# Performance work log

Hardware: AMD Instinct MI355X
Metric: run time of the kernel (lower is better)

The kernel has to match this reference:

```python
import jax, jax.numpy as jnp
import numpy as np

N = 50000        # nodes
E = 800000       # edges
E_PAIR = 200000  # pos/neg link pairs
IN = 256
HID = (512, 256, 160)
NEG_SLOPE = 0.2


def _lin_w(k, i, o):
    s = 1.0 / np.sqrt(i)
    return jax.random.uniform(k, (i, o), jnp.float32, -s, s)


def setup_inputs() -> dict:
    key = jax.random.key(0)
    ks = jax.random.split(key, 16)
    inp = {
        'x': jax.random.normal(ks[0], (N, IN), jnp.float32),
        'w': jax.random.uniform(ks[1], (E,), jnp.float32),
        'src': jax.random.randint(ks[2], (E,), 0, N),
        'dst': jax.random.randint(ks[3], (E,), 0, N),
        'pos_src': jax.random.randint(ks[4], (E_PAIR,), 0, N),
        'pos_dst': jax.random.randint(ks[5], (E_PAIR,), 0, N),
        'neg_src': jax.random.randint(ks[6], (E_PAIR,), 0, N),
        'neg_dst': jax.random.randint(ks[7], (E_PAIR,), 0, N),
        # GraphConv weights/biases
        'W1': _lin_w(ks[8], IN, HID[0]), 'b1': jnp.zeros((HID[0],), jnp.float32),
        'W2': _lin_w(ks[9], HID[0], HID[1]), 'b2': jnp.zeros((HID[1],), jnp.float32),
        'W3': _lin_w(ks[10], HID[1], HID[2]), 'b3': jnp.zeros((HID[2],), jnp.float32),
        # predictor MLP: 160 -> 80 -> 40 -> 1
        'P1': _lin_w(ks[11], HID[2], HID[2] // 2), 'pb1': jnp.zeros((HID[2] // 2,), jnp.float32),
        'P2': _lin_w(ks[12], HID[2] // 2, HID[2] // 4), 'pb2': jnp.zeros((HID[2] // 4,), jnp.float32),
        'P3': _lin_w(ks[13], HID[2] // 4, 1), 'pb3': jnp.zeros((1,), jnp.float32),
    }
    return inp


def _degree_norms(src, dst):
    ones = jnp.ones((E,), jnp.float32)
    out_deg = jnp.clip(jax.ops.segment_sum(ones, src, num_segments=N), 1.0)
    in_deg = jnp.clip(jax.ops.segment_sum(ones, dst, num_segments=N), 1.0)
    # norm='both': D_out^{-1/2} on source side, D_in^{-1/2} on dest side
    return (out_deg ** -0.5)[:, None], (in_deg ** -0.5)[:, None]


def _graph_conv(h, W, b, src, dst, w, out_norm, in_norm, project_first):
    # DGL GraphConv (norm='both', edge_weight=w): scale src feats, multiply
    # messages by edge weight, sum-aggregate, scale by in-degree norm, + bias.
    # DGL projects before aggregation iff in_feats > out_feats (same math).
    h = h * out_norm
    if project_first:
        h = h @ W
    agg = jax.ops.segment_sum(h[src] * w[:, None], dst, num_segments=N)
    if not project_first:
        agg = agg @ W
    return agg * in_norm + b


def _predictor(z, P1, pb1, P2, pb2, P3, pb3):
    z = jax.nn.leaky_relu(z @ P1 + pb1, NEG_SLOPE)
    z = jax.nn.leaky_relu(z @ P2 + pb2, NEG_SLOPE)
    return z @ P3 + pb3


def reference(x, w, src, dst, pos_src, pos_dst, neg_src, neg_dst,
              W1, b1, W2, b2, W3, b3, P1, pb1, P2, pb2, P3, pb3):
    out_norm, in_norm = _degree_norms(src, dst)
    h = _graph_conv(x, W1, b1, src, dst, w, out_norm, in_norm, project_first=False)  # 256<=512
    h = jax.nn.relu(h)
    h = _graph_conv(h, W2, b2, src, dst, w, out_norm, in_norm, project_first=True)   # 512>256
    h = jax.nn.relu(h)
    h = _graph_conv(h, W3, b3, src, dst, w, out_norm, in_norm, project_first=True)   # 256>160
    h_pos = _predictor(h[pos_src] * h[pos_dst], P1, pb1, P2, pb2, P3, pb3)
    h_neg = _predictor(h[neg_src] * h[neg_dst], P1, pb1, P2, pb2, P3, pb3)
    return h_pos, h_neg, h
```

## Files before the change

kernel.cpp:

```cpp
#include <hip/hip_runtime.h>
#include <math.h>

#define NN 50000
#define EE 800000
#define NPAIR 200000

typedef unsigned short u16;
typedef short short8v __attribute__((ext_vector_type(8)));
typedef float float16v __attribute__((ext_vector_type(16)));

__device__ __forceinline__ float leaky(float x){ return x >= 0.f ? x : 0.2f*x; }

__device__ __forceinline__ u16 bfhi(float x){
  union{float f; unsigned u;} v; v.f = x;
  unsigned r = (v.u + 0x7FFFu + ((v.u >> 16) & 1u)) >> 16;
  return (u16)r;
}
__device__ __forceinline__ float bf2f(u16 h){
  union{unsigned u; float f;} v; v.u = ((unsigned)h) << 16; return v.f;
}
__device__ __forceinline__ void split2(float x, float y, unsigned &hp, unsigned &lp){
  u16 hx = bfhi(x), hy = bfhi(y);
  u16 lx = bfhi(x - bf2f(hx)), ly = bfhi(y - bf2f(hy));
  hp = (unsigned)hx | ((unsigned)hy << 16);
  lp = (unsigned)lx | ((unsigned)ly << 16);
}


__global__ void degree_kernel(const int* __restrict__ src, const int* __restrict__ dst,
                              int* cnt_out, int* cnt_in){
  int i = blockIdx.x*blockDim.x + threadIdx.x;
  if(i < EE){
    atomicAdd(&cnt_out[src[i]], 1);
    atomicAdd(&cnt_in[dst[i]], 1);
  }
}

__global__ void norm_kernel(const int* __restrict__ cnt_out, const int* __restrict__ cnt_in,
                            float* __restrict__ out_norm, float* __restrict__ in_norm){
  int i = blockIdx.x*blockDim.x + threadIdx.x;
  if(i < NN){
    int o = cnt_out[i]; if(o < 1) o = 1;
    int d = cnt_in[i];  if(d < 1) d = 1;
    out_norm[i] = 1.f/sqrtf((float)o);
    in_norm[i]  = 1.f/sqrtf((float)d);
  }
}

__global__ void scan_kernel(const int* __restrict__ cnt, int* __restrict__ row_off){
  const int T = 512;
  __shared__ int sums[T];
  int t = threadIdx.x;
  int chunk = (NN + T - 1)/T;
  int base = t*chunk;
  int hi = base + chunk; if(hi > NN) hi = NN;
  int s = 0;
  for(int i = base; i < hi; i++) s += cnt[i];
  sums[t] = s;
  __syncthreads();
  for(int off = 1; off < T; off <<= 1){
    int add = (t >= off) ? sums[t-off] : 0;
    __syncthreads();
    sums[t] += add;
    __syncthreads();
  }
  int run = sums[t] - s;
  for(int i = base; i < hi; i++){ row_off[i] = run; run += cnt[i]; }
  if(t == T-1) row_off[NN] = EE;
}

__global__ void bucket_kernel(const int* __restrict__ src, const int* __restrict__ dst,
                              const float* __restrict__ w, const float* __restrict__ out_norm,
                              const int* __restrict__ row_off,
                              int* fill, int* __restrict__ es, float* __restrict__ ew){
  int i = blockIdx.x*blockDim.x + threadIdx.x;
  if(i < EE){
    int d = dst[i];
    int s = src[i];
    int p = row_off[d] + atomicAdd(&fill[d], 1);
    es[p] = s;
    ew[p] = w[i] * out_norm[s];
  }
}

__global__ void wsplit_kernel(const float* __restrict__ W, int K, int M,
                              u16* __restrict__ Whi, u16* __restrict__ Wlo){
  int i = blockIdx.x*256 + threadIdx.x;
  if(i < K*M){
    int m = i / K, k = i - m*K;
    float a = W[(size_t)k*M + m];
    u16 h = bfhi(a);
    Whi[i] = h;
    Wlo[i] = bfhi(a - bf2f(h));
  }
}

template<int F, int MODE>
__global__ __launch_bounds__(256) void agg_kernel(
    const float* __restrict__ feat, const int* __restrict__ es,
    const float* __restrict__ ew, const int* __restrict__ row_off,
    const float* __restrict__ innorm, const float* __restrict__ bias,
    float* __restrict__ out){
  constexpr int F4 = F/4;
  int wid = threadIdx.x >> 6, lane = threadIdx.x & 63;
  int v = blockIdx.x*4 + wid;
  if(v >= NN || lane >= F4) return;
  int s = row_off[v], e = row_off[v+1];
  const float4* f4 = (const float4*)feat;
  float4 a0 = {0,0,0,0}, a1 = {0,0,0,0}, a2 = {0,0,0,0}, a3 = {0,0,0,0};
  int j = s;
  for(; j + 3 < e; j += 4){
    int   i0 = es[j],   i1 = es[j+1], i2 = es[j+2], i3 = es[j+3];
    float w0 = ew[j],   w1 = ew[j+1], w2 = ew[j+2], w3 = ew[j+3];
    float4 r0 = f4[(size_t)i0*F4 + lane];
    float4 r1 = f4[(size_t)i1*F4 + lane];
    float4 r2 = f4[(size_t)i2*F4 + lane];
    float4 r3 = f4[(size_t)i3*F4 + lane];
    a0.x += r0.x*w0; a0.y += r0.y*w0; a0.z += r0.z*w0; a0.w += r0.w*w0;
    a1.x += r1.x*w1; a1.y += r1.y*w1; a1.z += r1.z*w1; a1.w += r1.w*w1;
    a2.x += r2.x*w2; a2.y += r2.y*w2; a2.z += r2.z*w2; a2.w += r2.w*w2;
    a3.x += r3.x*w3; a3.y += r3.y*w3; a3.z += r3.z*w3; a3.w += r3.w*w3;
  }
  for(; j < e; j++){
    int idx = es[j]; float wt = ew[j];
    float4 r = f4[(size_t)idx*F4 + lane];
    a0.x += r.x*wt; a0.y += r.y*wt; a0.z += r.z*wt; a0.w += r.w*wt;
  }
  float4 r;
  r.x = (a0.x+a1.x)+(a2.x+a3.x);
  r.y = (a0.y+a1.y)+(a2.y+a3.y);
  r.z = (a0.z+a1.z)+(a2.z+a3.z);
  r.w = (a0.w+a1.w)+(a2.w+a3.w);
  if(MODE >= 1){
    float inm = innorm[v];
    float4 bb = *(const float4*)&bias[lane*4];
    r.x = r.x*inm + bb.x; r.y = r.y*inm + bb.y;
    r.z = r.z*inm + bb.z; r.w = r.w*inm + bb.w;
    if(MODE == 1){
      r.x = fmaxf(r.x, 0.f); r.y = fmaxf(r.y, 0.f);
      r.z = fmaxf(r.z, 0.f); r.w = fmaxf(r.w, 0.f);
    }
  }
  ((float4*)(out + (size_t)v*F))[lane] = r;
}

template<bool EPI>
__global__ __launch_bounds__(256) void gemm_mfma(
    const float* __restrict__ A, const u16* __restrict__ Bhi, const u16* __restrict__ Blo,
    float* __restrict__ C, int K, int M,
    const float* __restrict__ innorm, const float* __restrict__ bias){
  __shared__ u16 sAhi[128*40];
  __shared__ u16 sAlo[128*40];
  __shared__ u16 sBhi[128*40];
  __shared__ u16 sBlo[128*40];
  int tid = threadIdx.x;
  int row0 = blockIdx.x*128, col0 = blockIdx.y*128;
  int wv = tid >> 6, L = tid & 63;
  int wr = (wv >> 1)*64, wc = (wv & 1)*64;
  int srow = tid >> 1, skh = (tid & 1)*16;

  float16v acc[2][2];
  #pragma unroll
  for(int i = 0; i < 2; i++)
    #pragma unroll
    for(int j = 0; j < 2; j++)
      #pragma unroll
      for(int r = 0; r < 16; r++) acc[i][j][r] = 0.f;

  const float* Arow = A + (size_t)(row0 + srow)*K;
  bool av = (row0 + srow) < NN;
  bool bv = (col0 + srow) < M;
  const u16* bhsrc = Bhi + (size_t)(col0 + srow)*K;
  const u16* blsrc = Blo + (size_t)(col0 + srow)*K;
  const uint4 z4 = make_uint4(0,0,0,0);

  for(int k0 = 0; k0 < K; k0 += 32){
    float4 af0 = {0,0,0,0}, af1 = {0,0,0,0}, af2 = {0,0,0,0}, af3 = {0,0,0,0};
    if(av){
      af0 = *(const float4*)&Arow[k0 + skh];
      af1 = *(const float4*)&Arow[k0 + skh + 4];
      af2 = *(const float4*)&Arow[k0 + skh + 8];
      af3 = *(const float4*)&Arow[k0 + skh + 12];
    }
    uint4 bh0 = z4, bh1 = z4, bl0 = z4, bl1 = z4;
    if(bv){
      bh0 = *(const uint4*)&bhsrc[k0 + skh];
      bh1 = *(const uint4*)&bhsrc[k0 + skh + 8];
      bl0 = *(const uint4*)&blsrc[k0 + skh];
      bl1 = *(const uint4*)&blsrc[k0 + skh + 8];
    }
    unsigned h0,h1,h2,h3,h4,h5,h6,h7, l0,l1,l2,l3,l4,l5,l6,l7;
    split2(af0.x, af0.y, h0, l0); split2(af0.z, af0.w, h1, l1);
    split2(af1.x, af1.y, h2, l2); split2(af1.z, af1.w, h3, l3);
    split2(af2.x, af2.y, h4, l4); split2(af2.z, af2.w, h5, l5);
    split2(af3.x, af3.y, h6, l6); split2(af3.z, af3.w, h7, l7);
    __syncthreads();
    int sa = srow*40 + skh;
    *(uint4*)&sAhi[sa]     = make_uint4(h0,h1,h2,h3);
    *(uint4*)&sAhi[sa + 8] = make_uint4(h4,h5,h6,h7);
    *(uint4*)&sAlo[sa]     = make_uint4(l0,l1,l2,l3);
    *(uint4*)&sAlo[sa + 8] = make_uint4(l4,l5,l6,l7);
    *(uint4*)&sBhi[sa]     = bh0;
    *(uint4*)&sBhi[sa + 8] = bh1;
    *(uint4*)&sBlo[sa]     = bl0;
    *(uint4*)&sBlo[sa + 8] = bl1;
    __syncthreads();
    #pragma unroll
    for(int ks = 0; ks < 2; ks++){
      int ko = ks*16 + (L >> 5)*8;
      int ra0 = (wr + (L & 31))*40 + ko, ra1 = ra0 + 32*40;
      int rb0 = (wc + (L & 31))*40 + ko, rb1 = rb0 + 32*40;
      short8v ah0 = *(const short8v*)&sAhi[ra0];
      short8v ah1 = *(const short8v*)&sAhi[ra1];
      short8v al0 = *(const short8v*)&sAlo[ra0];
      short8v al1 = *(const short8v*)&sAlo[ra1];
      short8v bhf0 = *(const short8v*)&sBhi[rb0];
      short8v bhf1 = *(const short8v*)&sBhi[rb1];
      short8v blf0 = *(const short8v*)&sBlo[rb0];
      short8v blf1 = *(const short8v*)&sBlo[rb1];
      acc[0][0] = __builtin_amdgcn_mfma_f32_32x32x16_bf16(ah0, bhf0, acc[0][0], 0,0,0);
      acc[0][0] = __builtin_amdgcn_mfma_f32_32x32x16_bf16(al0, bhf0, acc[0][0], 0,0,0);
      acc[0][0] = __builtin_amdgcn_mfma_f32_32x32x16_bf16(ah0, blf0, acc[0][0], 0,0,0);
      acc[0][1] = __builtin_amdgcn_mfma_f32_32x32x16_bf16(ah0, bhf1, acc[0][1], 0,0,0);
      acc[0][1] = __builtin_amdgcn_mfma_f32_32x32x16_bf16(al0, bhf1, acc[0][1], 0,0,0);
      acc[0][1] = __builtin_amdgcn_mfma_f32_32x32x16_bf16(ah0, blf1, acc[0][1], 0,0,0);
      acc[1][0] = __builtin_amdgcn_mfma_f32_32x32x16_bf16(ah1, bhf0, acc[1][0], 0,0,0);
      acc[1][0] = __builtin_amdgcn_mfma_f32_32x32x16_bf16(al1, bhf0, acc[1][0], 0,0,0);
      acc[1][0] = __builtin_amdgcn_mfma_f32_32x32x16_bf16(ah1, blf0, acc[1][0], 0,0,0);
      acc[1][1] = __builtin_amdgcn_mfma_f32_32x32x16_bf16(ah1, bhf1, acc[1][1], 0,0,0);
      acc[1][1] = __builtin_amdgcn_mfma_f32_32x32x16_bf16(al1, bhf1, acc[1][1], 0,0,0);
      acc[1][1] = __builtin_amdgcn_mfma_f32_32x32x16_bf16(ah1, blf1, acc[1][1], 0,0,0);
    }
  }

  int cB = L & 31, rq = 4*(L >> 5);
  #pragma unroll
  for(int tr = 0; tr < 2; tr++){
    #pragma unroll
    for(int tc = 0; tc < 2; tc++){
      int c = col0 + wc + tc*32 + cB;
      if(c >= M) continue;
      #pragma unroll
      for(int reg = 0; reg < 16; reg++){
        int r = row0 + wr + tr*32 + (reg & 3) + 8*(reg >> 2) + rq;
        if(r >= NN) continue;
        float v = acc[tr][tc][reg];
        if(EPI) v = fmaxf(v*innorm[r] + bias[c], 0.f);
        C[(size_t)r*M + c] = v;
      }
    }
  }
}

#define ZS 68
__global__ __launch_bounds__(256) void predictor_kernel(
    const float* __restrict__ h3, const int* __restrict__ ps, const int* __restrict__ pd,
    const int* __restrict__ ns, const int* __restrict__ nd,
    const float* __restrict__ P1, const float* __restrict__ pb1,
    const float* __restrict__ P2, const float* __restrict__ pb2,
    const float* __restrict__ P3, const float* __restrict__ pb3,
    float* __restrict__ out){
  __shared__ float smem[13440];
  float* z   = smem;
  float* p1p = smem + 160*ZS;
  float* y1  = smem;
  float* p2  = smem + 5200;
  float* y2  = smem + 8400;
  int tid = threadIdx.x;
  int pair0 = blockIdx.x*64;

  {
    int p = tid >> 2, sub = tid & 3;
    int q = pair0 + p;
    int a, b;
    if(q < NPAIR){ a = ps[q]; b = pd[q]; }
    else         { a = ns[q-NPAIR]; b = nd[q-NPAIR]; }
    const float4* ra = (const float4*)(h3 + (size_t)a*160);
    const float4* rb = (const float4*)(h3 + (size_t)b*160);
    #pragma unroll
    for(int it = 0; it < 10; it++){
      int g = sub + it*4;
      float4 va = ra[g], vb = rb[g];
      int k = g*4;
      z[(k+0)*ZS + p] = va.x*vb.x;
      z[(k+1)*ZS + p] = va.y*vb.y;
      z[(k+2)*ZS + p] = va.z*vb.z;
      z[(k+3)*ZS + p] = va.w*vb.w;
    }
  }

  int tr = tid >> 4, tc = tid & 15;
  float acc1[4][5];
  #pragma unroll
  for(int j = 0; j < 5; j++){
    float bv = pb1[tc + 16*j];
    #pragma unroll
    for(int i = 0; i < 4; i++) acc1[i][j] = bv;
  }
  for(int k0 = 0; k0 < 160; k0 += 32){
    __syncthreads();
    const float4* gp = (const float4*)(P1 + k0*80);
    for(int i = tid; i < 640; i += 256) ((float4*)p1p)[i] = gp[i];
    __syncthreads();
    #pragma unroll 8
    for(int kk = 0; kk < 32; kk++){
      float4 av = *(const float4*)&z[(k0+kk)*ZS + tr*4];
      float a0 = av.x, a1 = av.y, a2 = av.z, a3 = av.w;
      float b[5];
      #pragma unroll
      for(int j = 0; j < 5; j++) b[j] = p1p[kk*80 + tc + 16*j];
      #pragma unroll
      for(int j = 0; j < 5; j++){
        acc1[0][j] += a0*b[j];
        acc1[1][j] += a1*b[j];
        acc1[2][j] += a2*b[j];
        acc1[3][j] += a3*b[j];
      }
    }
  }
  __syncthreads();

  #pragma unroll
  for(int i = 0; i < 4; i++)
    #pragma unroll
    for(int j = 0; j < 5; j++)
      y1[(tc + 16*j)*65 + tr*4 + i] = leaky(acc1[i][j]);
  for(int i = tid; i < 800; i += 256) ((float4*)p2)[i] = ((const float4*)P2)[i];
  __syncthreads();

  int tr2 = tid >> 3, tc2 = tid & 7;
  float acc2[2][5];
  #pragma unroll
  for(int j = 0; j < 5; j++){
    float bv = pb2[tc2 + 8*j];
    acc2[0][j] = bv; acc2[1][j] = bv;
  }
  #pragma unroll 4
  for(int k = 0; k < 80; k++){
    float a0 = y1[k*65 + tr2*2], a1 = y1[k*65 + tr2*2 + 1];
    #pragma unroll
    for(int j = 0; j < 5; j++){
      float bv = p2[k*40 + tc2 + 8*j];
      acc2[0][j] += a0*bv;
      acc2[1][j] += a1*bv;
    }
  }
  #pragma unroll
  for(int i = 0; i < 2; i++)
    #pragma unroll
    for(int j = 0; j < 5; j++)
      y2[(tc2 + 8*j)*65 + tr2*2 + i] = leaky(acc2[i][j]);
  __syncthreads();

  if(tid < 64){
    float s = pb3[0];
    #pragma unroll 8
    for(int k = 0; k < 40; k++) s += y2[k*65 + tid]*P3[k];
    out[pair0 + tid] = s;
  }
}


extern "C" void kernel_launch(void* const* d_in, const int* in_sizes, int n_in,
                              void* d_out, int out_size, void* d_ws, size_t ws_size,
                              hipStream_t stream) {
  const float* x  = (const float*)d_in[0];
  const float* w  = (const float*)d_in[1];
  const int* src  = (const int*)d_in[2];
  const int* dst  = (const int*)d_in[3];
  const int* ps   = (const int*)d_in[4];
  const int* pd   = (const int*)d_in[5];
  const int* ns   = (const int*)d_in[6];
  const int* nd   = (const int*)d_in[7];
  const float* W1 = (const float*)d_in[8];  const float* b1  = (const float*)d_in[9];
  const float* W2 = (const float*)d_in[10]; const float* b2  = (const float*)d_in[11];
  const float* W3 = (const float*)d_in[12]; const float* b3  = (const float*)d_in[13];
  const float* P1 = (const float*)d_in[14]; const float* pb1 = (const float*)d_in[15];
  const float* P2 = (const float*)d_in[16]; const float* pb2 = (const float*)d_in[17];
  const float* P3 = (const float*)d_in[18]; const float* pb3 = (const float*)d_in[19];
  float* out = (float*)d_out;

  char* p = (char*)d_ws;
  auto alloc = [&](size_t bytes)->char*{
    char* r = p; p += (bytes + 255) & ~(size_t)255; return r;
  };
  int*   cnt_out = (int*)  alloc(NN*4);
  int*   cnt_in  = (int*)  alloc(NN*4);
  int*   fill    = (int*)  alloc(NN*4);
  int*   row_off = (int*)  alloc((NN+1)*4);
  float* out_nrm = (float*)alloc(NN*4);
  float* in_nrm  = (float*)alloc(NN*4);
  int*   es      = (int*)  alloc((size_t)EE*4);
  float* ew      = (float*)alloc((size_t)EE*4);
  u16*   w1h     = (u16*)  alloc(256*512*2);
  u16*   w1l     = (u16*)  alloc(256*512*2);
  u16*   w2h     = (u16*)  alloc(512*256*2);
  u16*   w2l     = (u16*)  alloc(512*256*2);
  u16*   w3h     = (u16*)  alloc(256*160*2);
  u16*   w3l     = (u16*)  alloc(256*160*2);
  float* bufA    = (float*)alloc((size_t)NN*512*4);
  float* bufB    = (float*)alloc((size_t)NN*256*4);
  float* bufC    = (float*)alloc((size_t)NN*256*4);

  size_t cntPad = (NN*4 + 255) & ~(size_t)255;
  hipMemsetAsync(cnt_out, 0, 3*cntPad, stream);

  degree_kernel<<<(EE+255)/256, 256, 0, stream>>>(src, dst, cnt_out, cnt_in);
  norm_kernel<<<(NN+255)/256, 256, 0, stream>>>(cnt_out, cnt_in, out_nrm, in_nrm);
  scan_kernel<<<1, 512, 0, stream>>>(cnt_in, row_off);
  bucket_kernel<<<(EE+255)/256, 256, 0, stream>>>(src, dst, w, out_nrm, row_off, fill, es, ew);
  wsplit_kernel<<<512, 256, 0, stream>>>(W1, 256, 512, w1h, w1l);
  wsplit_kernel<<<512, 256, 0, stream>>>(W2, 512, 256, w2h, w2l);
  wsplit_kernel<<<160, 256, 0, stream>>>(W3, 256, 160, w3h, w3l);

  int aggGrid = (NN + 3)/4;

  agg_kernel<256,0><<<aggGrid, 256, 0, stream>>>(x, es, ew, row_off, nullptr, nullptr, bufC);
  gemm_mfma<true><<<dim3(391,4), 256, 0, stream>>>(bufC, w1h, w1l, bufA, 256, 512, in_nrm, b1);

  gemm_mfma<false><<<dim3(391,2), 256, 0, stream>>>(bufA, w2h, w2l, bufB, 512, 256, nullptr, nullptr);
  agg_kernel<256,1><<<aggGrid, 256, 0, stream>>>(bufB, es, ew, row_off, in_nrm, b2, bufC);

  gemm_mfma<false><<<dim3(391,2), 256, 0, stream>>>(bufC, w3h, w3l, bufB, 256, 160, nullptr, nullptr);
  agg_kernel<160,2><<<aggGrid, 256, 0, stream>>>(bufB, es, ew, row_off, in_nrm, b3, out + 2*NPAIR);

  predictor_kernel<<<(2*NPAIR)/64, 256, 0, stream>>>(out + 2*NPAIR, ps, pd, ns, nd,
                                                     P1, pb1, P2, pb2, P3, pb3, out);
}
```

Before: 1.042 ms.

## Move predictor MLP onto bf16x3 split MFMA matrix cores

Rewrites the link predictor's first two layers to use 32x32x16 bf16 MFMA with hi/lo split operands (three products per step) instead of scalar FP32 FMAs. P1 and P2 are pre-split and transposed into padded bf16 buffers by a new setup kernel. The last layer is folded into a lane-shuffle reduction. This aims to cut ALU time in the predictor, at the cost of extra split and convert work, some padded waste, and a small loss of precision.

```diff
diff --git a/kernel.cpp b/kernel.cpp
--- a/kernel.cpp
+++ b/kernel.cpp
@@ -25,6 +25,7 @@
   hp = (unsigned)hx | ((unsigned)hy << 16);
   lp = (unsigned)lx | ((unsigned)ly << 16);
 }
+#define MFMA_BF16 __builtin_amdgcn_mfma_f32_32x32x16_bf16
 
 
 __global__ void degree_kernel(const int* __restrict__ src, const int* __restrict__ dst,
@@ -92,6 +93,24 @@
     u16 h = bfhi(a);
     Whi[i] = h;
     Wlo[i] = bfhi(a - bf2f(h));
+  }
+}
+
+__global__ void psplit_kernel(const float* __restrict__ P1, const float* __restrict__ P2,
+                              u16* __restrict__ P1th, u16* __restrict__ P1tl,
+                              u16* __restrict__ P2th, u16* __restrict__ P2tl){
+  int i = blockIdx.x*256 + threadIdx.x;
+  if(i < 96*160){
+    int c = i/160, k = i - c*160;
+    float v = (c < 80) ? P1[k*80 + c] : 0.f;
+    u16 h = bfhi(v);
+    P1th[i] = h; P1tl[i] = bfhi(v - bf2f(h));
+  }
+  if(i < 64*80){
+    int c = i/80, k = i - c*80;
+    float v = (c < 40) ? P2[k*40 + c] : 0.f;
+    u16 h = bfhi(v);
+    P2th[i] = h; P2tl[i] = bfhi(v - bf2f(h));
   }
 }
 
@@ -218,18 +237,18 @@
       short8v bhf1 = *(const short8v*)&sBhi[rb1];
       short8v blf0 = *(const short8v*)&sBlo[rb0];
       short8v blf1 = *(const short8v*)&sBlo[rb1];
-      acc[0][0] = __builtin_amdgcn_mfma_f32_32x32x16_bf16(ah0, bhf0, acc[0][0], 0,0,0);
-      acc[0][0] = __builtin_amdgcn_mfma_f32_32x32x16_bf16(al0, bhf0, acc[0][0], 0,0,0);
-      acc[0][0] = __builtin_amdgcn_mfma_f32_32x32x16_bf16(ah0, blf0, acc[0][0], 0,0,0);
-      acc[0][1] = __builtin_amdgcn_mfma_f32_32x32x16_bf16(ah0, bhf1, acc[0][1], 0,0,0);
-      acc[0][1] = __builtin_amdgcn_mfma_f32_32x32x16_bf16(al0, bhf1, acc[0][1], 0,0,0);
-      acc[0][1] = __builtin_amdgcn_mfma_f32_32x32x16_bf16(ah0, blf1, acc[0][1], 0,0,0);
-      acc[1][0] = __builtin_amdgcn_mfma_f32_32x32x16_bf16(ah1, bhf0, acc[1][0], 0,0,0);
-      acc[1][0] = __builtin_amdgcn_mfma_f32_32x32x16_bf16(al1, bhf0, acc[1][0], 0,0,0);
-      acc[1][0] = __builtin_amdgcn_mfma_f32_32x32x16_bf16(ah1, blf0, acc[1][0], 0,0,0);
-      acc[1][1] = __builtin_amdgcn_mfma_f32_32x32x16_bf16(ah1, bhf1, acc[1][1], 0,0,0);
-      acc[1][1] = __builtin_amdgcn_mfma_f32_32x32x16_bf16(al1, bhf1, acc[1][1], 0,0,0);
-      acc[1][1] = __builtin_amdgcn_mfma_f32_32x32x16_bf16(ah1, blf1, acc[1][1], 0,0,0);
+      acc[0][0] = MFMA_BF16(ah0, bhf0, acc[0][0], 0,0,0);
+      acc[0][0] = MFMA_BF16(al0, bhf0, acc[0][0], 0,0,0);
+      acc[0][0] = MFMA_BF16(ah0, blf0, acc[0][0], 0,0,0);
+      acc[0][1] = MFMA_BF16(ah0, bhf1, acc[0][1], 0,0,0);
+      acc[0][1] = MFMA_BF16(al0, bhf1, acc[0][1], 0,0,0);
+      acc[0][1] = MFMA_BF16(ah0, blf1, acc[0][1], 0,0,0);
+      acc[1][0] = MFMA_BF16(ah1, bhf0, acc[1][0], 0,0,0);
+      acc[1][0] = MFMA_BF16(al1, bhf0, acc[1][0], 0,0,0);
+      acc[1][0] = MFMA_BF16(ah1, blf0, acc[1][0], 0,0,0);
+      acc[1][1] = MFMA_BF16(ah1, bhf1, acc[1][1], 0,0,0);
+      acc[1][1] = MFMA_BF16(al1, bhf1, acc[1][1], 0,0,0);
+      acc[1][1] = MFMA_BF16(ah1, blf1, acc[1][1], 0,0,0);
     }
   }
 
@@ -252,22 +271,34 @@
   }
 }
 
-#define ZS 68
-__global__ __launch_bounds__(256) void predictor_kernel(
-    const float* __restrict__ h3, const int* __restrict__ ps, const int* __restrict__ pd,
+#define ZSTR 168
+#define P1STR 24
+#define Y1STR 88
+__global__ __launch_bounds__(256) void predictor_mfma(
+    const float* __restrict__ h3,
+    const int* __restrict__ ps, const int* __restrict__ pd,
     const int* __restrict__ ns, const int* __restrict__ nd,
-    const float* __restrict__ P1, const float* __restrict__ pb1,
-    const float* __restrict__ P2, const float* __restrict__ pb2,
+    const u16* __restrict__ P1th, const u16* __restrict__ P1tl,
+    const float* __restrict__ pb1,
+    const u16* __restrict__ P2th, const u16* __restrict__ P2tl,
+    const float* __restrict__ pb2,
     const float* __restrict__ P3, const float* __restrict__ pb3,
     float* __restrict__ out){
-  __shared__ float smem[13440];
-  float* z   = smem;
-  float* p1p = smem + 160*ZS;
-  float* y1  = smem;
-  float* p2  = smem + 5200;
-  float* y2  = smem + 8400;
+  __shared__ u16 smem[26112];
+  u16* zh  = smem;
+  u16* zl  = smem + 64*ZSTR;
+  u16* p1h = smem + 2*64*ZSTR;
+  u16* p1l = p1h + 96*P1STR;
+  u16* y1h = smem;
+  u16* y1l = smem + 64*Y1STR;
+  u16* p2h = smem + 2*64*Y1STR;
+  u16* p2l = smem + 3*64*Y1STR;
+  float* part = (float*)(smem + 4*64*Y1STR);
+
   int tid = threadIdx.x;
   int pair0 = blockIdx.x*64;
+  int w = tid >> 6, L = tid & 63;
+  int lrow = L & 31, lk = (L >> 5)*8;
 
   {
     int p = tid >> 2, sub = tid & 3;
@@ -281,83 +312,122 @@
     for(int it = 0; it < 10; it++){
       int g = sub + it*4;
       float4 va = ra[g], vb = rb[g];
-      int k = g*4;
-      z[(k+0)*ZS + p] = va.x*vb.x;
-      z[(k+1)*ZS + p] = va.y*vb.y;
-      z[(k+2)*ZS + p] = va.z*vb.z;
-      z[(k+3)*ZS + p] = va.w*vb.w;
-    }
-  }
-
-  int tr = tid >> 4, tc = tid & 15;
-  float acc1[4][5];
+      unsigned hp0, lp0, hp1, lp1;
+      split2(va.x*vb.x, va.y*vb.y, hp0, lp0);
+      split2(va.z*vb.z, va.w*vb.w, hp1, lp1);
+      *(uint2*)&zh[p*ZSTR + 4*g] = make_uint2(hp0, hp1);
+      *(uint2*)&zl[p*ZSTR + 4*g] = make_uint2(lp0, lp1);
+    }
+  }
+
+  float16v acc1a, acc1b;
   #pragma unroll
-  for(int j = 0; j < 5; j++){
-    float bv = pb1[tc + 16*j];
+  for(int r = 0; r < 16; r++){ acc1a[r] = 0.f; acc1b[r] = 0.f; }
+  int j1 = w, j2 = (w < 2) ? (w + 4) : -1;
+  int pt1 = j1/3, ct1 = j1 - pt1*3;
+  int pt2 = (j2 >= 0) ? j2/3 : 0;
+  int ct2j = (j2 >= 0) ? (j2 - pt2*3) : 0;
+
+  for(int k0 = 0; k0 < 160; k0 += 16){
+    __syncthreads();
+    if(tid < 192){
+      int c = tid >> 1, half = tid & 1;
+      uint4 vh = *(const uint4*)&P1th[c*160 + k0 + half*8];
+      uint4 vl = *(const uint4*)&P1tl[c*160 + k0 + half*8];
+      *(uint4*)&p1h[c*P1STR + half*8] = vh;
+      *(uint4*)&p1l[c*P1STR + half*8] = vl;
+    }
+    __syncthreads();
+    {
+      short8v ah = *(const short8v*)&zh[(pt1*32 + lrow)*ZSTR + k0 + lk];
+      short8v al = *(const short8v*)&zl[(pt1*32 + lrow)*ZSTR + k0 + lk];
+      short8v bh = *(const short8v*)&p1h[(ct1*32 + lrow)*P1STR + lk];
+      short8v bl = *(const short8v*)&p1l[(ct1*32 + lrow)*P1STR + lk];
+      acc1a = MFMA_BF16(ah, bh, acc1a, 0,0,0);
+      acc1a = MFMA_BF16(al, bh, acc1a, 0,0,0);
+      acc1a = MFMA_BF16(ah, bl, acc1a, 0,0,0);
+    }
+    if(j2 >= 0){
+      short8v ah = *(const short8v*)&zh[(pt2*32 + lrow)*ZSTR + k0 + lk];
+      short8v al = *(const short8v*)&zl[(pt2*32 + lrow)*ZSTR + k0 + lk];
+      short8v bh = *(const short8v*)&p1h[(ct2j*32 + lrow)*P1STR + lk];
+      short8v bl = *(const short8v*)&p1l[(ct2j*32 + lrow)*P1STR + lk];
+      acc1b = MFMA_BF16(ah, bh, acc1b, 0,0,0);
+      acc1b = MFMA_BF16(al, bh, acc1b, 0,0,0);
+      acc1b = MFMA_BF16(ah, bl, acc1b, 0,0,0);
+    }
+  }
+  __syncthreads();
+
+  {
+    int c = ct1*32 + lrow;
+    if(c < 80){
+      float pb = pb1[c];
+      #pragma unroll
+      for(int r = 0; r < 16; r++){
+        int p = pt1*32 + (r & 3) + 8*(r >> 2) + 4*(L >> 5);
+        float v = leaky(acc1a[r] + pb);
+        u16 h = bfhi(v);
+        y1h[p*Y1STR + c] = h;
+        y1l[p*Y1STR + c] = bfhi(v - bf2f(h));
+      }
+    }
+  }
+  if(j2 >= 0){
+    int c = ct2j*32 + lrow;
+    if(c < 80){
+      float pb = pb1[c];
+      #pragma unroll
+      for(int r = 0; r < 16; r++){
+        int p = pt2*32 + (r & 3) + 8*(r >> 2) + 4*(L >> 5);
+        float v = leaky(acc1b[r] + pb);
+        u16 h = bfhi(v);
+        y1h[p*Y1STR + c] = h;
+        y1l[p*Y1STR + c] = bfhi(v - bf2f(h));
+      }
+    }
+  }
+  for(int i = tid; i < 640; i += 256){
+    int c = i/10, jj = i - c*10;
+    *(uint4*)&p2h[c*Y1STR + jj*8] = *(const uint4*)&P2th[c*80 + jj*8];
+    *(uint4*)&p2l[c*Y1STR + jj*8] = *(const uint4*)&P2tl[c*80 + jj*8];
+  }
+  __syncthreads();
+
+  float16v acc2;
+  #pragma unroll
+  for(int r = 0; r < 16; r++) acc2[r] = 0.f;
+  int pt = w & 1, c2t = w >> 1;
+  for(int k0 = 0; k0 < 80; k0 += 16){
+    short8v ah = *(const short8v*)&y1h[(pt*32 + lrow)*Y1STR + k0 + lk];
+    short8v al = *(const short8v*)&y1l[(pt*32 + lrow)*Y1STR + k0 + lk];
+    short8v bh = *(const short8v*)&p2h[(c2t*32 + lrow)*Y1STR + k0 + lk];
+    short8v bl = *(const short8v*)&p2l[(c2t*32 + lrow)*Y1STR + k0 + lk];
+    acc2 = MFMA_BF16(ah, bh, acc2, 0,0,0);
+    acc2 = MFMA_BF16(al, bh, acc2, 0,0,0);
+    acc2 = MFMA_BF16(ah, bl, acc2, 0,0,0);
+  }
+
+  int c2 = c2t*32 + lrow;
+  float pb2c = (c2 < 40) ? pb2[c2] : 0.f;
+  float p3c  = (c2 < 40) ? P3[c2]  : 0.f;
+  float vals[16];
+  #pragma unroll
+  for(int r = 0; r < 16; r++){
+    float v = leaky(acc2[r] + pb2c) * p3c;
     #pragma unroll
-    for(int i = 0; i < 4; i++) acc1[i][j] = bv;
-  }
-  for(int k0 = 0; k0 < 160; k0 += 32){
-    __syncthreads();
-    const float4* gp = (const float4*)(P1 + k0*80);
-    for(int i = tid; i < 640; i += 256) ((float4*)p1p)[i] = gp[i];
-    __syncthreads();
-    #pragma unroll 8
-    for(int kk = 0; kk < 32; kk++){
-      float4 av = *(const float4*)&z[(k0+kk)*ZS + tr*4];
-      float a0 = av.x, a1 = av.y, a2 = av.z, a3 = av.w;
-      float b[5];
-      #pragma unroll
-      for(int j = 0; j < 5; j++) b[j] = p1p[kk*80 + tc + 16*j];
-      #pragma unroll
-      for(int j = 0; j < 5; j++){
-        acc1[0][j] += a0*b[j];
-        acc1[1][j] += a1*b[j];
-        acc1[2][j] += a2*b[j];
-        acc1[3][j] += a3*b[j];
-      }
+    for(int m = 1; m < 32; m <<= 1) v += __shfl_xor(v, m);
+    vals[r] = v;
+  }
+  if(lrow == 0){
+    #pragma unroll
+    for(int r = 0; r < 16; r++){
+      int p = pt*32 + (r & 3) + 8*(r >> 2) + 4*(L >> 5);
+      part[c2t*64 + p] = vals[r];
     }
   }
   __syncthreads();
-
-  #pragma unroll
-  for(int i = 0; i < 4; i++)
-    #pragma unroll
-    for(int j = 0; j < 5; j++)
-      y1[(tc + 16*j)*65 + tr*4 + i] = leaky(acc1[i][j]);
-  for(int i = tid; i < 800; i += 256) ((float4*)p2)[i] = ((const float4*)P2)[i];
-  __syncthreads();
-
-  int tr2 = tid >> 3, tc2 = tid & 7;
-  float acc2[2][5];
-  #pragma unroll
-  for(int j = 0; j < 5; j++){
-    float bv = pb2[tc2 + 8*j];
-    acc2[0][j] = bv; acc2[1][j] = bv;
-  }
-  #pragma unroll 4
-  for(int k = 0; k < 80; k++){
-    float a0 = y1[k*65 + tr2*2], a1 = y1[k*65 + tr2*2 + 1];
-    #pragma unroll
-    for(int j = 0; j < 5; j++){
-      float bv = p2[k*40 + tc2 + 8*j];
-      acc2[0][j] += a0*bv;
-      acc2[1][j] += a1*bv;
-    }
-  }
-  #pragma unroll
-  for(int i = 0; i < 2; i++)
-    #pragma unroll
-    for(int j = 0; j < 5; j++)
-      y2[(tc2 + 8*j)*65 + tr2*2 + i] = leaky(acc2[i][j]);
-  __syncthreads();
-
-  if(tid < 64){
-    float s = pb3[0];
-    #pragma unroll 8
-    for(int k = 0; k < 40; k++) s += y2[k*65 + tid]*P3[k];
-    out[pair0 + tid] = s;
-  }
+  if(tid < 64) out[pair0 + tid] = (part[tid] + part[64 + tid]) + pb3[0];
 }
 
 
@@ -398,6 +468,10 @@
   u16*   w2l     = (u16*)  alloc(512*256*2);
   u16*   w3h     = (u16*)  alloc(256*160*2);
   u16*   w3l     = (u16*)  alloc(256*160*2);
+  u16*   p1th    = (u16*)  alloc(96*160*2);
+  u16*   p1tl    = (u16*)  alloc(96*160*2);
+  u16*   p2th    = (u16*)  alloc(64*80*2);
+  u16*   p2tl    = (u16*)  alloc(64*80*2);
   float* bufA    = (float*)alloc((size_t)NN*512*4);
   float* bufB    = (float*)alloc((size_t)NN*256*4);
   float* bufC    = (float*)alloc((size_t)NN*256*4);
@@ -412,6 +486,7 @@
   wsplit_kernel<<<512, 256, 0, stream>>>(W1, 256, 512, w1h, w1l);
   wsplit_kernel<<<512, 256, 0, stream>>>(W2, 512, 256, w2h, w2l);
   wsplit_kernel<<<160, 256, 0, stream>>>(W3, 256, 160, w3h, w3l);
+  psplit_kernel<<<60, 256, 0, stream>>>(P1, P2, p1th, p1tl, p2th, p2tl);
 
   int aggGrid = (NN + 3)/4;
 
@@ -424,6 +499,7 @@
   gemm_mfma<false><<<dim3(391,2), 256, 0, stream>>>(bufC, w3h, w3l, bufB, 256, 160, nullptr, nullptr);
   agg_kernel<160,2><<<aggGrid, 256, 0, stream>>>(bufB, es, ew, row_off, in_nrm, b3, out + 2*NPAIR);
 
-  predictor_kernel<<<(2*NPAIR)/64, 256, 0, stream>>>(out + 2*NPAIR, ps, pd, ns, nd,
-                                                     P1, pb1, P2, pb2, P3, pb3, out);
-}
+  predictor_mfma<<<(2*NPAIR)/64, 256, 0, stream>>>(out + 2*NPAIR, ps, pd, ns, nd,
+                                                   p1th, p1tl, pb1, p2th, p2tl, pb2,
+                                                   P3, pb3, out);
+}
```

New measurement: 944.3 us. -9.4%, faster.
